# Optimization experiments

Measured on AMD Instinct MI355X. Metric: run time of the kernel, lower is better.

Reference implementation:

```python
import jax, jax.numpy as jnp
import numpy as np

N = 50000
E = 800000
IN_C, HID_C, OUT_C = 512, 128, 64


def setup_inputs() -> dict:
    key = jax.random.key(0)
    k = jax.random.split(key, 8)
    x = jax.random.normal(k[0], (N, IN_C), dtype=jnp.float32)
    edge_index = jax.random.randint(k[1], (2, E), 0, N, dtype=jnp.int64)
    edge_weight = jax.random.uniform(k[2], (E,), dtype=jnp.float32)
    # GCNConv parameters (glorot-like init)
    W1 = jax.random.normal(k[3], (IN_C, HID_C), dtype=jnp.float32) * (1.0 / np.sqrt(IN_C))
    b1 = jnp.zeros((HID_C,), dtype=jnp.float32)
    W2 = jax.random.normal(k[4], (HID_C, OUT_C), dtype=jnp.float32) * (1.0 / np.sqrt(HID_C))
    b2 = jnp.zeros((OUT_C,), dtype=jnp.float32)
    return {"x": x, "edge_index": edge_index, "edge_weight": edge_weight,
            "W1": W1, "b1": b1, "W2": W2, "b2": b2}


def _add_self_loops(edge_index, edge_weight, num_nodes):
    loop = jnp.arange(num_nodes, dtype=edge_index.dtype)
    ei = jnp.concatenate([edge_index, jnp.stack([loop, loop])], axis=1)
    ew = jnp.concatenate([edge_weight, jnp.ones((num_nodes,), edge_weight.dtype)])
    return ei, ew


def _gcn_conv(x, row, col, norm, W, b, num_nodes):
    # linear transform first (PyG GCNConv), then normalized scatter-add aggregation
    xw = x @ W                                    # [N, F_out]
    msg = norm[:, None] * xw[row]                 # gather + scale, [E', F_out]
    out = jnp.zeros((num_nodes, xw.shape[1]), xw.dtype).at[col].add(msg)
    return out + b


def reference(x, edge_index, edge_weight, W1, b1, W2, b2):
    num_nodes = x.shape[0]
    ei, ew = _add_self_loops(edge_index, edge_weight, num_nodes)
    row, col = ei[0], ei[1]
    # symmetric normalization: D^{-1/2} A D^{-1/2} (deg over destination index)
    deg = jnp.zeros((num_nodes,), ew.dtype).at[col].add(ew)
    dinv = jnp.where(deg > 0, jax.lax.rsqrt(deg), 0.0)
    norm = dinv[row] * ew * dinv[col]
    h = _gcn_conv(x, row, col, norm, W1, b1, num_nodes)
    h = jax.nn.relu(h)
    # dropout p=0.5 is identity in eval mode
    return _gcn_conv(h, row, col, norm, W2, b2, num_nodes)
```

## Files before the change

### kernel.cpp

```cpp
#include <hip/hip_runtime.h>

#define NNODES 50000
#define NEDGES 800000
#define IN_C   512
#define HID_C  128
#define OUT_C  64
#define NBUCK  196
#define BCAP   5120
#define BREG   5376

typedef float  f32x4  __attribute__((ext_vector_type(4)));
typedef __bf16 bf16x8 __attribute__((ext_vector_type(8)));
typedef short  short8 __attribute__((ext_vector_type(8)));

#define GLDS(src, dst) \
  __builtin_amdgcn_global_load_lds( \
      (const __attribute__((address_space(1))) unsigned int*)(src), \
      (__attribute__((address_space(3))) unsigned int*)(dst), 16, 0, 0)

__device__ __forceinline__ float bf2f(unsigned short u) {
  unsigned int x = (unsigned int)u << 16;
  return __builtin_bit_cast(float, x);
}
__device__ __forceinline__ unsigned short f16bits(float f) {
  _Float16 h = (_Float16)f;
  return __builtin_bit_cast(unsigned short, h);
}
__device__ __forceinline__ float f16val(unsigned short u) {
  return (float)__builtin_bit_cast(_Float16, u);
}


__device__ __forceinline__ void wsplit_one(const float* __restrict__ W,
                                           unsigned short* __restrict__ Th,
                                           unsigned short* __restrict__ Tl,
                                           int K, int N, int id) {
  int k = id % K, n = id / K;
  float f = W[(size_t)k * N + n];
  __bf16 hb = (__bf16)f;
  __bf16 lb = (__bf16)(f - (float)hb);
  Th[id] = __builtin_bit_cast(unsigned short, hb);
  Tl[id] = __builtin_bit_cast(unsigned short, lb);
}

__global__ void __launch_bounds__(256) prep0_kernel(
    unsigned int* __restrict__ gclaim,
    const float* __restrict__ W1, unsigned short* __restrict__ W1th,
    unsigned short* __restrict__ W1tl,
    const float* __restrict__ W2, unsigned short* __restrict__ W2th,
    unsigned short* __restrict__ W2tl) {
  int id = blockIdx.x * blockDim.x + threadIdx.x;
  if (id < 256) { if (id < NBUCK) gclaim[id] = (unsigned int)id * BCAP; return; }
  int s = id - 256;
  if (s < IN_C * HID_C) wsplit_one(W1, W1th, W1tl, IN_C, HID_C, s);
  else if (s < IN_C * HID_C + HID_C * OUT_C)
    wsplit_one(W2, W2th, W2tl, HID_C, OUT_C, s - IN_C * HID_C);
}

template <int K, int N, int WR, int WC>
__device__ __forceinline__ void gemm_body(const float* __restrict__ X,
                                          const unsigned short* __restrict__ Bth,
                                          unsigned short* __restrict__ Y, int M, int bid) {
  constexpr int NW = WR * WC;
  constexpr int BM = WR * 32;
  constexpr int NI = K / 32;
  constexpr int ASLOTS = (BM / 8) / NW;
  constexpr int BSLOTS = (N / 16) / NW;

  __shared__ float          As[2][BM * 32];
  __shared__ unsigned short Bs[2][N * 32];

  int tid = threadIdx.x;
  int lane = tid & 63, wid = tid >> 6;
  int wr = wid / WC, wc = wid % WC;
  int row0blk = bid * BM;
  int row0 = row0blk + wr * 32;
  int rlo = lane & 15;
  int khi = lane >> 4;

  f32x4 acc[2][4] = {};

  auto stage = [&](int t, int buf) {
    int kb = t * 32;
#pragma unroll
    for (int i = 0; i < ASLOTS; ++i) {
      int slot = wid * ASLOTS + i;
      int rt = slot * 8 + (lane >> 3);
      int gr = row0blk + rt; gr = gr < M ? gr : M - 1;
      int gs = (lane & 7) ^ (lane >> 3);
      GLDS(X + (size_t)gr * K + kb + gs * 4, &As[buf][slot * 256]);
    }
#pragma unroll
    for (int i = 0; i < BSLOTS; ++i) {
      int slot = wid * BSLOTS + i;
      int c = slot * 16 + (lane >> 2);
      int gs = (lane & 3) ^ (lane >> 4);
      GLDS(Bth + (size_t)c * K + kb + gs * 8, &Bs[buf][slot * 512]);
    }
  };

  stage(0, 0);
  __syncthreads();

#pragma unroll 1
  for (int t = 0; t < NI; ++t) {
    int buf = t & 1;
    if (t + 1 < NI) stage(t + 1, buf ^ 1);

    bf16x8 ah[2], al[2];
#pragma unroll
    for (int m = 0; m < 2; ++m) {
      int rt = wr * 32 + m * 16 + rlo;
      int p0 = (khi * 2) ^ (rlo & 7), p1 = (khi * 2 + 1) ^ (rlo & 7);
      f32x4 v0 = *reinterpret_cast<const f32x4*>(&As[buf][rt * 32 + p0 * 4]);
      f32x4 v1 = *reinterpret_cast<const f32x4*>(&As[buf][rt * 32 + p1 * 4]);
      float f[8] = {v0.x, v0.y, v0.z, v0.w, v1.x, v1.y, v1.z, v1.w};
#pragma unroll
      for (int i = 0; i < 8; ++i) {
        __bf16 hv = (__bf16)f[i];
        ah[m][i] = hv;
        al[m][i] = (__bf16)(f[i] - (float)hv);
      }
    }
    short8 bh[4];
#pragma unroll
    for (int n = 0; n < 4; ++n) {
      int c = wc * 64 + n * 16 + rlo;
      int pos = khi ^ (rlo >> 2);
      bh[n] = *reinterpret_cast<const short8*>(&Bs[buf][c * 32 + pos * 8]);
    }
#pragma unroll
    for (int m = 0; m < 2; ++m)
#pragma unroll
      for (int n = 0; n < 4; ++n)
        acc[m][n] = __builtin_amdgcn_mfma_f32_16x16x32_bf16(
            ah[m], __builtin_bit_cast(bf16x8, bh[n]), acc[m][n], 0, 0, 0);
#pragma unroll
    for (int m = 0; m < 2; ++m)
#pragma unroll
      for (int n = 0; n < 4; ++n)
        acc[m][n] = __builtin_amdgcn_mfma_f32_16x16x32_bf16(
            al[m], __builtin_bit_cast(bf16x8, bh[n]), acc[m][n], 0, 0, 0);
    __syncthreads();
  }

#pragma unroll
  for (int m = 0; m < 2; ++m)
#pragma unroll
    for (int j = 0; j < 4; ++j) {
      int row = row0 + m * 16 + khi * 4 + j;
      if (row < M) {
#pragma unroll
        for (int n = 0; n < 4; ++n) {
          __bf16 q = (__bf16)acc[m][n][j];
          Y[(size_t)row * N + wc * 64 + n * 16 + rlo] = __builtin_bit_cast(unsigned short, q);
        }
      }
    }
}

__global__ void __launch_bounds__(512, 4) fused_gemm1_scatter_kernel(
    const float* __restrict__ X, const unsigned short* __restrict__ Bth,
    unsigned short* __restrict__ Y, int M,
    int ngemm, const int* __restrict__ ei, const float* __restrict__ ew,
    unsigned int* __restrict__ gclaim, unsigned long long* __restrict__ binned, int nE) {
  if ((int)blockIdx.x < ngemm) {
    gemm_body<IN_C, HID_C, 4, 2>(X, Bth, Y, M, blockIdx.x);
    return;
  }
  __shared__ unsigned int h[NBUCK];
  __shared__ unsigned int cur[NBUCK];
  int t = threadIdx.x;
  if (t < NBUCK) h[t] = 0;
  __syncthreads();
  int base = ((int)blockIdx.x - ngemm) * 4096;
  int r[8]; unsigned int c[8]; unsigned short wb[8];
#pragma unroll
  for (int i = 0; i < 8; ++i) {
    int e = base + i * 512 + t;
    if (e < nE) {
      r[i] = ei[e];
      c[i] = (unsigned int)ei[nE + e];
      wb[i] = f16bits(ew[e]);
      atomicAdd(&h[c[i] >> 8], 1u);
    } else {
      c[i] = 0xFFFFFFFFu;
    }
  }
  __syncthreads();
  if (t < NBUCK) cur[t] = h[t] ? atomicAdd(&gclaim[t], h[t]) : 0u;
  __syncthreads();
#pragma unroll
  for (int i = 0; i < 8; ++i) {
    if (c[i] != 0xFFFFFFFFu) {
      unsigned int pos = atomicAdd(&cur[c[i] >> 8], 1u);
      unsigned long long rec = (unsigned long long)((unsigned int)r[i] & 0xFFFFu)
                             | ((unsigned long long)(c[i] & 0xFFu) << 16)
                             | ((unsigned long long)wb[i] << 32);
      binned[pos] = rec;
    }
  }
}

__global__ void __launch_bounds__(256) bucket_build_kernel(
    const unsigned long long* __restrict__ binned, const unsigned int* __restrict__ gclaim,
    float* __restrict__ dinv, int* __restrict__ offs, unsigned short* __restrict__ cnts,
    unsigned int* __restrict__ edges) {
  int b = blockIdx.x, t = threadIdx.x;
  int base = b * BCAP;
  int cnt = (int)gclaim[b] - base;
  int nb = min(256, NNODES - b * 256);
  int csrbase = b * BREG;
  __shared__ unsigned int ec[256], wf[256], cur[256];
  __shared__ int sc[256];
  __shared__ unsigned int image[BREG];
  ec[t] = 0; wf[t] = 0;
  __syncthreads();
  for (int i = t; i < cnt; i += 256) {
    unsigned long long rec = binned[base + i];
    int dlo = (int)((rec >> 16) & 255ULL);
    atomicAdd(&ec[dlo], 1u);
    float w = f16val((unsigned short)(rec >> 32));
    atomicAdd(&wf[dlo], (unsigned int)(w * 1048576.0f + 0.5f));
  }
  __syncthreads();
  int cn = (t < nb) ? (int)ec[t] + 1 : 0;
  sc[t] = cn;
  __syncthreads();
  for (int off = 1; off < 256; off <<= 1) {
    int u = (t >= off) ? sc[t - off] : 0;
    __syncthreads();
    sc[t] += u;
    __syncthreads();
  }
  if (t < nb) {
    float deg = (float)wf[t] * (1.0f / 1048576.0f) + 1.0f;
    int g = b * 256 + t;
    float di = rsqrtf(deg);
    dinv[g] = di;
    int loc = sc[t] - cn;
    offs[g] = csrbase + loc;
    cnts[g] = (unsigned short)ec[t];
    cur[t] = (unsigned int)(loc + 1);
    image[loc] = (unsigned int)g | (0x3C00u << 16);
  }
  __syncthreads();
  for (int i = t; i < cnt; i += 256) {
    unsigned long long rec = binned[base + i];
    int src = (int)(rec & 0xFFFFULL);
    int dlo = (int)((rec >> 16) & 255ULL);
    unsigned int wb = (unsigned int)((rec >> 32) & 0xFFFFULL);
    unsigned int pos = atomicAdd(&cur[dlo], 1u);
    image[pos] = (unsigned int)src | (wb << 16);
  }
  __syncthreads();
  int total = cnt + nb;
  for (int j = t; j < total; j += 256) edges[csrbase + j] = image[j];
}

template <int K, int N, int WR, int WC>
__global__ void __launch_bounds__(WR * WC * 64, 4) gemm_bf16a_kernel(
    const unsigned short* __restrict__ X, const unsigned short* __restrict__ Bth,
    const unsigned short* __restrict__ Btl, unsigned short* __restrict__ Y, int M) {
  constexpr int NW = WR * WC;
  constexpr int BM = WR * 32;
  constexpr int NI = K / 32;
  constexpr int ASLOTS = (BM / 16) / NW;
  constexpr int BSLOTS = (N / 8) / NW;

  __shared__ unsigned short As[2][BM * 32];
  __shared__ unsigned short Bs[2][2][N * 32];

  int tid = threadIdx.x;
  int lane = tid & 63, wid = tid >> 6;
  int wr = wid / WC, wc = wid % WC;
  int row0blk = blockIdx.x * BM;
  int row0 = row0blk + wr * 32;
  int rlo = lane & 15;
  int khi = lane >> 4;

  f32x4 acc[2][4] = {};

  auto stage = [&](int t, int buf) {
    int kb = t * 32;
#pragma unroll
    for (int i = 0; i < ASLOTS; ++i) {
      int slot = wid * ASLOTS + i;
      int rt = slot * 16 + (lane >> 2);
      int gr = row0blk + rt; gr = gr < M ? gr : M - 1;
      int gs = (lane & 3) ^ ((lane >> 3) & 3);
      GLDS(X + (size_t)gr * K + kb + gs * 8, &As[buf][slot * 512]);
    }
#pragma unroll
    for (int i = 0; i < BSLOTS; ++i) {
      int slot = wid * BSLOTS + i;
      int half = slot / (N / 16);
      int idx = slot % (N / 16);
      const unsigned short* Wt = half ? Btl : Bth;
      int c = idx * 16 + (lane >> 2);
      int gs = (lane & 3) ^ (lane >> 4);
      GLDS(Wt + (size_t)c * K + kb + gs * 8, &Bs[buf][half][idx * 512]);
    }
  };

  stage(0, 0);
  __syncthreads();

#pragma unroll 1
  for (int t = 0; t < NI; ++t) {
    int buf = t & 1;
    if (t + 1 < NI) stage(t + 1, buf ^ 1);

    short8 ah[2];
#pragma unroll
    for (int m = 0; m < 2; ++m) {
      int rt = wr * 32 + m * 16 + rlo;
      int g = khi ^ ((rt >> 1) & 3);
      ah[m] = *reinterpret_cast<const short8*>(&As[buf][rt * 32 + g * 8]);
    }
    short8 bh[4], bl[4];
#pragma unroll
    for (int n = 0; n < 4; ++n) {
      int c = wc * 64 + n * 16 + rlo;
      int pos = khi ^ (rlo >> 2);
      bh[n] = *reinterpret_cast<const short8*>(&Bs[buf][0][c * 32 + pos * 8]);
      bl[n] = *reinterpret_cast<const short8*>(&Bs[buf][1][c * 32 + pos * 8]);
    }
#pragma unroll
    for (int m = 0; m < 2; ++m)
#pragma unroll
      for (int n = 0; n < 4; ++n)
        acc[m][n] = __builtin_amdgcn_mfma_f32_16x16x32_bf16(
            __builtin_bit_cast(bf16x8, ah[m]), __builtin_bit_cast(bf16x8, bh[n]),
            acc[m][n], 0, 0, 0);
#pragma unroll
    for (int m = 0; m < 2; ++m)
#pragma unroll
      for (int n = 0; n < 4; ++n)
        acc[m][n] = __builtin_amdgcn_mfma_f32_16x16x32_bf16(
            __builtin_bit_cast(bf16x8, ah[m]), __builtin_bit_cast(bf16x8, bl[n]),
            acc[m][n], 0, 0, 0);
    __syncthreads();
  }

#pragma unroll
  for (int m = 0; m < 2; ++m)
#pragma unroll
    for (int j = 0; j < 4; ++j) {
      int row = row0 + m * 16 + khi * 4 + j;
      if (row < M) {
#pragma unroll
        for (int n = 0; n < 4; ++n) {
          __bf16 q = (__bf16)acc[m][n][j];
          Y[(size_t)row * N + wc * 64 + n * 16 + rlo] = __builtin_bit_cast(unsigned short, q);
        }
      }
    }
}

template <int F, bool RELU, bool OUTBF>
__global__ void __launch_bounds__(256) agg_kernel(const unsigned short* __restrict__ feat,
                                                  const int* __restrict__ offs,
                                                  const unsigned short* __restrict__ cnts,
                                                  const unsigned int* __restrict__ edges,
                                                  const float* __restrict__ dinv,
                                                  const float* __restrict__ bias,
                                                  void* __restrict__ outv, int n) {
  constexpr int LPN = F / 8;
  constexpr int NPW = 64 / LPN;
  constexpr int NPB = 4 * NPW;
  int wid = threadIdx.x >> 6;
  int lane = threadIdx.x & 63;
  int node = blockIdx.x * NPB + wid * NPW + lane / LPN;
  int lf = (lane % LPN) * 8;
  if (node >= n) return;
  int e0 = offs[node];
  int e1 = e0 + 1 + (int)cnts[node];

  float acc[8] = {};

  auto fmaEdge = [&](unsigned int q) {
    int row = (int)(q & 0xFFFFu);
    float w = f16val((unsigned short)(q >> 16)) * dinv[row];
    short8 v = *reinterpret_cast<const short8*>(&feat[(size_t)row * F + lf]);
#pragma unroll
    for (int j = 0; j < 8; ++j)
      acc[j] = fmaf(w, bf2f((unsigned short)v[j]), acc[j]);
  };

  int e = e0;
  for (; e + 4 <= e1; e += 4) {
    unsigned int q0 = edges[e], q1 = edges[e + 1], q2 = edges[e + 2], q3 = edges[e + 3];
    fmaEdge(q0); fmaEdge(q1); fmaEdge(q2); fmaEdge(q3);
  }
  for (; e < e1; ++e) fmaEdge(edges[e]);

  float dd = dinv[node];
#pragma unroll
  for (int j = 0; j < 8; ++j) {
    acc[j] = fmaf(acc[j], dd, bias[lf + j]);
    if (RELU) acc[j] = fmaxf(acc[j], 0.f);
  }
  if constexpr (OUTBF) {
    short8 o;
#pragma unroll
    for (int j = 0; j < 8; ++j) {
      __bf16 q = (__bf16)acc[j];
      o[j] = (short)__builtin_bit_cast(unsigned short, q);
    }
    *reinterpret_cast<short8*>((unsigned short*)outv + (size_t)node * F + lf) = o;
  } else {
    float* out = (float*)outv;
    float4 o0 = make_float4(acc[0], acc[1], acc[2], acc[3]);
    float4 o1 = make_float4(acc[4], acc[5], acc[6], acc[7]);
    *reinterpret_cast<float4*>(&out[(size_t)node * F + lf]) = o0;
    *reinterpret_cast<float4*>(&out[(size_t)node * F + lf + 4]) = o1;
  }
}


extern "C" void kernel_launch(void* const* d_in, const int* in_sizes, int n_in,
                              void* d_out, int out_size, void* d_ws, size_t ws_size,
                              hipStream_t stream) {
  const float* x  = (const float*)d_in[0];
  const int*   ei = (const int*)d_in[1];
  const float* ew = (const float*)d_in[2];
  const float* W1 = (const float*)d_in[3];
  const float* b1 = (const float*)d_in[4];
  const float* W2 = (const float*)d_in[5];
  const float* b2 = (const float*)d_in[6];
  float* out = (float*)d_out;

  const int N = NNODES, E = NEDGES;

  char* p = (char*)d_ws;
  auto alloc = [&](size_t bytes) { char* r = p; p += (bytes + 255) & ~(size_t)255; return r; };
  unsigned int* gclaim = (unsigned int*)alloc(256 * 4);
  float* dinv   = (float*)alloc((size_t)N * 4);
  int*   offs   = (int*)  alloc((size_t)N * 4);
  unsigned short* cnts = (unsigned short*)alloc((size_t)N * 2);
  unsigned long long* binned = (unsigned long long*)alloc((size_t)NBUCK * BCAP * 8);
  unsigned int* edges  = (unsigned int*)alloc((size_t)NBUCK * BREG * 4);
  unsigned short* xw = (unsigned short*)alloc((size_t)N * HID_C * 2);
  unsigned short* h  = (unsigned short*)alloc((size_t)N * HID_C * 2);
  unsigned short* W1th = (unsigned short*)alloc((size_t)IN_C * HID_C * 2);
  unsigned short* W1tl = (unsigned short*)alloc((size_t)IN_C * HID_C * 2);
  unsigned short* W2th = (unsigned short*)alloc((size_t)HID_C * OUT_C * 2);
  unsigned short* W2tl = (unsigned short*)alloc((size_t)HID_C * OUT_C * 2);

  const int PREP0 = 256 + IN_C * HID_C + HID_C * OUT_C;
  prep0_kernel<<<(PREP0 + 255) / 256, 256, 0, stream>>>(
      gclaim, W1, W1th, W1tl, W2, W2th, W2tl);

  const int NGEMM = (N + 127) / 128;
  const int NSCAT = (E + 4095) / 4096;
  fused_gemm1_scatter_kernel<<<NGEMM + NSCAT, 512, 0, stream>>>(
      x, W1th, xw, N, NGEMM, ei, ew, gclaim, binned, E);

  bucket_build_kernel<<<NBUCK, 256, 0, stream>>>(binned, gclaim, dinv, offs, cnts, edges);

  agg_kernel<HID_C, true, true><<<(N + 15) / 16, 256, 0, stream>>>(
      xw, offs, cnts, edges, dinv, b1, h, N);

  gemm_bf16a_kernel<HID_C, OUT_C, 8, 1><<<(N + 255) / 256, 512, 0, stream>>>(h, W2th, W2tl, xw, N);
  agg_kernel<OUT_C, false, false><<<(N + 31) / 32, 256, 0, stream>>>(
      xw, offs, cnts, edges, dinv, b2, out, N);
}
```

Measured before the change: 102.8 us.

## Move edge binning to its own kernel and fuse bucket build with GEMM1

```diff
diff --git a/kernel.cpp b/kernel.cpp
--- a/kernel.cpp
+++ b/kernel.cpp
@@ -57,8 +57,45 @@
     wsplit_one(W2, W2th, W2tl, HID_C, OUT_C, s - IN_C * HID_C);
 }
 
+__global__ void __launch_bounds__(1024) bin_scatter_kernel(
+    const int* __restrict__ ei, const float* __restrict__ ew,
+    unsigned int* __restrict__ gclaim, unsigned long long* __restrict__ binned, int nE) {
+  __shared__ unsigned int h[NBUCK];
+  __shared__ unsigned int cur[NBUCK];
+  int t = threadIdx.x;
+  if (t < NBUCK) h[t] = 0;
+  __syncthreads();
+  int base = (int)blockIdx.x * 8192;
+  int r[8]; unsigned int c[8]; unsigned short wb[8];
+#pragma unroll
+  for (int i = 0; i < 8; ++i) {
+    int e = base + i * 1024 + t;
+    if (e < nE) {
+      r[i] = ei[e];
+      c[i] = (unsigned int)ei[nE + e];
+      wb[i] = f16bits(ew[e]);
+      atomicAdd(&h[c[i] >> 8], 1u);
+    } else {
+      c[i] = 0xFFFFFFFFu;
+    }
+  }
+  __syncthreads();
+  if (t < NBUCK) cur[t] = h[t] ? atomicAdd(&gclaim[t], h[t]) : 0u;
+  __syncthreads();
+#pragma unroll
+  for (int i = 0; i < 8; ++i) {
+    if (c[i] != 0xFFFFFFFFu) {
+      unsigned int pos = atomicAdd(&cur[c[i] >> 8], 1u);
+      unsigned long long rec = (unsigned long long)((unsigned int)r[i] & 0xFFFFu)
+                             | ((unsigned long long)(c[i] & 0xFFu) << 16)
+                             | ((unsigned long long)wb[i] << 32);
+      binned[pos] = rec;
+    }
+  }
+}
+
 template <int K, int N, int WR, int WC>
-__device__ __forceinline__ void gemm_body(const float* __restrict__ X,
+__device__ __forceinline__ void gemm_body(char* smem, const float* __restrict__ X,
                                           const unsigned short* __restrict__ Bth,
                                           unsigned short* __restrict__ Y, int M, int bid) {
   constexpr int NW = WR * WC;
@@ -67,8 +104,8 @@
   constexpr int ASLOTS = (BM / 8) / NW;
   constexpr int BSLOTS = (N / 16) / NW;
 
-  __shared__ float          As[2][BM * 32];
-  __shared__ unsigned short Bs[2][N * 32];
+  float          (*As)[BM * 32] = reinterpret_cast<float(*)[BM * 32]>(smem);
+  unsigned short (*Bs)[N * 32]  = reinterpret_cast<unsigned short(*)[N * 32]>(smem + 2 * BM * 32 * 4);
 
   int tid = threadIdx.x;
   int lane = tid & 63, wid = tid >> 6;
@@ -159,64 +196,25 @@
     }
 }
 
-__global__ void __launch_bounds__(512, 4) fused_gemm1_scatter_kernel(
-    const float* __restrict__ X, const unsigned short* __restrict__ Bth,
-    unsigned short* __restrict__ Y, int M,
-    int ngemm, const int* __restrict__ ei, const float* __restrict__ ew,
-    unsigned int* __restrict__ gclaim, unsigned long long* __restrict__ binned, int nE) {
-  if ((int)blockIdx.x < ngemm) {
-    gemm_body<IN_C, HID_C, 4, 2>(X, Bth, Y, M, blockIdx.x);
-    return;
-  }
-  __shared__ unsigned int h[NBUCK];
-  __shared__ unsigned int cur[NBUCK];
-  int t = threadIdx.x;
-  if (t < NBUCK) h[t] = 0;
-  __syncthreads();
-  int base = ((int)blockIdx.x - ngemm) * 4096;
-  int r[8]; unsigned int c[8]; unsigned short wb[8];
-#pragma unroll
-  for (int i = 0; i < 8; ++i) {
-    int e = base + i * 512 + t;
-    if (e < nE) {
-      r[i] = ei[e];
-      c[i] = (unsigned int)ei[nE + e];
-      wb[i] = f16bits(ew[e]);
-      atomicAdd(&h[c[i] >> 8], 1u);
-    } else {
-      c[i] = 0xFFFFFFFFu;
-    }
-  }
-  __syncthreads();
-  if (t < NBUCK) cur[t] = h[t] ? atomicAdd(&gclaim[t], h[t]) : 0u;
-  __syncthreads();
-#pragma unroll
-  for (int i = 0; i < 8; ++i) {
-    if (c[i] != 0xFFFFFFFFu) {
-      unsigned int pos = atomicAdd(&cur[c[i] >> 8], 1u);
-      unsigned long long rec = (unsigned long long)((unsigned int)r[i] & 0xFFFFu)
-                             | ((unsigned long long)(c[i] & 0xFFu) << 16)
-                             | ((unsigned long long)wb[i] << 32);
-      binned[pos] = rec;
-    }
-  }
-}
-
-__global__ void __launch_bounds__(256) bucket_build_kernel(
+__device__ __forceinline__ void build_body(char* smem,
     const unsigned long long* __restrict__ binned, const unsigned int* __restrict__ gclaim,
     float* __restrict__ dinv, int* __restrict__ offs, unsigned short* __restrict__ cnts,
-    unsigned int* __restrict__ edges) {
-  int b = blockIdx.x, t = threadIdx.x;
+    unsigned int* __restrict__ edges, int b) {
+  unsigned int* ec    = (unsigned int*)smem;
+  unsigned int* wf    = ec + 256;
+  unsigned int* cur   = wf + 256;
+  int*          sc    = (int*)(cur + 256);
+  unsigned int* image = (unsigned int*)(sc + 256);
+
+  int t = threadIdx.x;
   int base = b * BCAP;
   int cnt = (int)gclaim[b] - base;
   int nb = min(256, NNODES - b * 256);
   int csrbase = b * BREG;
-  __shared__ unsigned int ec[256], wf[256], cur[256];
-  __shared__ int sc[256];
-  __shared__ unsigned int image[BREG];
-  ec[t] = 0; wf[t] = 0;
-  __syncthreads();
-  for (int i = t; i < cnt; i += 256) {
+
+  if (t < 256) { ec[t] = 0; wf[t] = 0; }
+  __syncthreads();
+  for (int i = t; i < cnt; i += 512) {
     unsigned long long rec = binned[base + i];
     int dlo = (int)((rec >> 16) & 255ULL);
     atomicAdd(&ec[dlo], 1u);
@@ -225,12 +223,12 @@
   }
   __syncthreads();
   int cn = (t < nb) ? (int)ec[t] + 1 : 0;
-  sc[t] = cn;
+  if (t < 256) sc[t] = cn;
   __syncthreads();
   for (int off = 1; off < 256; off <<= 1) {
-    int u = (t >= off) ? sc[t - off] : 0;
+    int u = (t < 256 && t >= off) ? sc[t - off] : 0;
     __syncthreads();
-    sc[t] += u;
+    if (t < 256) sc[t] += u;
     __syncthreads();
   }
   if (t < nb) {
@@ -245,7 +243,7 @@
     image[loc] = (unsigned int)g | (0x3C00u << 16);
   }
   __syncthreads();
-  for (int i = t; i < cnt; i += 256) {
+  for (int i = t; i < cnt; i += 512) {
     unsigned long long rec = binned[base + i];
     int src = (int)(rec & 0xFFFFULL);
     int dlo = (int)((rec >> 16) & 255ULL);
@@ -255,7 +253,20 @@
   }
   __syncthreads();
   int total = cnt + nb;
-  for (int j = t; j < total; j += 256) edges[csrbase + j] = image[j];
+  for (int j = t; j < total; j += 512) edges[csrbase + j] = image[j];
+}
+
+__global__ void __launch_bounds__(512, 4) fused_build_gemm1_kernel(
+    const float* __restrict__ X, const unsigned short* __restrict__ Bth,
+    unsigned short* __restrict__ Y, int M,
+    const unsigned long long* __restrict__ binned, const unsigned int* __restrict__ gclaim,
+    float* __restrict__ dinv, int* __restrict__ offs, unsigned short* __restrict__ cnts,
+    unsigned int* __restrict__ edges) {
+  __shared__ char smem[49152];
+  if ((int)blockIdx.x < NBUCK)
+    build_body(smem, binned, gclaim, dinv, offs, cnts, edges, (int)blockIdx.x);
+  else
+    gemm_body<IN_C, HID_C, 4, 2>(smem, X, Bth, Y, M, (int)blockIdx.x - NBUCK);
 }
 
 template <int K, int N, int WR, int WC>
@@ -452,12 +463,11 @@
   prep0_kernel<<<(PREP0 + 255) / 256, 256, 0, stream>>>(
       gclaim, W1, W1th, W1tl, W2, W2th, W2tl);
 
+  bin_scatter_kernel<<<(E + 8191) / 8192, 1024, 0, stream>>>(ei, ew, gclaim, binned, E);
+
   const int NGEMM = (N + 127) / 128;
-  const int NSCAT = (E + 4095) / 4096;
-  fused_gemm1_scatter_kernel<<<NGEMM + NSCAT, 512, 0, stream>>>(
-      x, W1th, xw, N, NGEMM, ei, ew, gclaim, binned, E);
-
-  bucket_build_kernel<<<NBUCK, 256, 0, stream>>>(binned, gclaim, dinv, offs, cnts, edges);
+  fused_build_gemm1_kernel<<<NBUCK + NGEMM, 512, 0, stream>>>(
+      x, W1th, xw, N, binned, gclaim, dinv, offs, cnts, edges);
 
   agg_kernel<HID_C, true, true><<<(N + 15) / 16, 256, 0, stream>>>(
       xw, offs, cnts, edges, dinv, b1, h, N);
```

After: 106.9 us. 3.9% more time.
